# Optimization experiments

Measured on AMD Instinct MI355X. Metric: run time of the kernel, lower is better.

## Reference

```python
import jax, jax.numpy as jnp
import numpy as np

C = 256          # in_channels == out_channels
K = 4            # number of parallel depthwise kernels
RED = 4          # SE reduction
KS = 3           # kernel size


def setup_inputs() -> dict:
    key = jax.random.key(0)
    ks = jax.random.split(key, 6)
    B, H, W = 32, 64, 64
    x = jax.random.normal(ks[0], (B, C, H, W), dtype=jnp.float32)
    # K depthwise kernels; per-conv torch weight shape = (C, 1, 3, 3)
    conv_w = jax.random.normal(ks[1], (K, C, 1, KS, KS), dtype=jnp.float32) * 0.1
    fc1_w = jax.random.normal(ks[2], (C // RED, C), dtype=jnp.float32) * (1.0 / np.sqrt(C))
    fc1_b = jnp.zeros((C // RED,), dtype=jnp.float32)
    fc2_w = jax.random.normal(ks[3], (K, C // RED), dtype=jnp.float32) * (1.0 / np.sqrt(C // RED))
    fc2_b = jnp.zeros((K,), dtype=jnp.float32)
    return {"x": x, "conv_w": conv_w, "fc1_w": fc1_w, "fc1_b": fc1_b,
            "fc2_w": fc2_w, "fc2_b": fc2_b}


def reference(x, conv_w, fc1_w, fc1_b, fc2_w, fc2_b):
    B, c, H, W = x.shape
    # --- attention branch: GAP -> fc -> relu -> fc -> softmax over K ---
    g = jnp.mean(x, axis=(2, 3))                       # [B, C]
    h = jax.nn.relu(g @ fc1_w.T + fc1_b)               # [B, C//r]
    attn = jax.nn.softmax(h @ fc2_w.T + fc2_b, axis=1) # [B, K]
    # --- all K depthwise convs as ONE grouped conv with K*C output channels ---
    # group i (input channel i) produces output channels [i*K:(i+1)*K],
    # so arrange weights as (C, K, 1, ks, ks) -> (C*K, 1, ks, ks)
    w_all = jnp.transpose(conv_w, (1, 0, 2, 3, 4)).reshape(c * K, 1, KS, KS)
    out = jax.lax.conv_general_dilated(
        x, w_all, window_strides=(1, 1), padding=[(1, 1), (1, 1)],
        feature_group_count=c,
        dimension_numbers=("NCHW", "OIHW", "NCHW"))    # [B, C*K, H, W]
    out = out.reshape(B, c, K, H, W)
    # attention-weighted sum over the K kernels
    return jnp.einsum("bckhw,bk->bchw", out, attn)
```

## Files before the change

kernel.cpp:

```cpp
#include <hip/hip_runtime.h>

#define CH 256
#define KK 4
#define HW 64
#define PLANE 4096
#define TILE_W 66

__global__ void gap_kernel(const float* __restrict__ x, float* __restrict__ g) {
    int plane = blockIdx.x;
    const float4* p = (const float4*)(x + (size_t)plane * PLANE);
    float sum = 0.f;
    for (int i = threadIdx.x; i < PLANE / 4; i += 256) {
        float4 v = p[i];
        sum += (v.x + v.y) + (v.z + v.w);
    }
    for (int off = 32; off > 0; off >>= 1)
        sum += __shfl_down(sum, off);
    __shared__ float ws[4];
    int lane = threadIdx.x & 63;
    int wid  = threadIdx.x >> 6;
    if (lane == 0) ws[wid] = sum;
    __syncthreads();
    if (threadIdx.x == 0)
        g[plane] = (ws[0] + ws[1] + ws[2] + ws[3]) * (1.f / PLANE);
}

__global__ void attn_kernel(const float* __restrict__ g,
                            const float* __restrict__ fc1_w, const float* __restrict__ fc1_b,
                            const float* __restrict__ fc2_w, const float* __restrict__ fc2_b,
                            float* __restrict__ attn) {
    int b = blockIdx.x;
    int t = threadIdx.x;
    __shared__ float gs[CH];
    __shared__ float h[64];
    __shared__ float logit[KK];
    for (int i = t; i < CH; i += 64) gs[i] = g[b * CH + i];
    __syncthreads();
    float acc = fc1_b[t];
    const float* wrow = fc1_w + t * CH;
    for (int i = 0; i < CH; ++i) acc = fmaf(wrow[i], gs[i], acc);
    h[t] = fmaxf(acc, 0.f);
    __syncthreads();
    if (t < KK) {
        float a = fc2_b[t];
        const float* w2 = fc2_w + t * 64;
        for (int i = 0; i < 64; ++i) a = fmaf(w2[i], h[i], a);
        logit[t] = a;
    }
    __syncthreads();
    if (t == 0) {
        float m = fmaxf(fmaxf(logit[0], logit[1]), fmaxf(logit[2], logit[3]));
        float e[KK];
        float s = 0.f;
        for (int k = 0; k < KK; ++k) { e[k] = expf(logit[k] - m); s += e[k]; }
        float inv = 1.f / s;
        for (int k = 0; k < KK; ++k) attn[b * KK + k] = e[k] * inv;
    }
}

__global__ void dwconv_kernel(const float* __restrict__ x, const float* __restrict__ conv_w,
                              const float* __restrict__ attn, float* __restrict__ out) {
    int plane = blockIdx.x;
    int b = plane >> 8;
    int c = plane & (CH - 1);
    __shared__ float tile[TILE_W * TILE_W];

    const float* xp = x + (size_t)plane * PLANE;
    for (int i = threadIdx.x; i < TILE_W * TILE_W; i += 256) {
        int sy = i / TILE_W;
        int sx = i - sy * TILE_W;
        int gy = sy - 1, gx = sx - 1;
        float v = 0.f;
        if ((unsigned)gy < 64u && (unsigned)gx < 64u) v = xp[(gy << 6) + gx];
        tile[i] = v;
    }

    float a0 = attn[b * KK + 0], a1 = attn[b * KK + 1],
          a2 = attn[b * KK + 2], a3 = attn[b * KK + 3];
    float w[9];
    #pragma unroll
    for (int j = 0; j < 9; ++j) {
        w[j] = a0 * conv_w[(0 * CH + c) * 9 + j]
             + a1 * conv_w[(1 * CH + c) * 9 + j]
             + a2 * conv_w[(2 * CH + c) * 9 + j]
             + a3 * conv_w[(3 * CH + c) * 9 + j];
    }
    __syncthreads();

    float* op = out + (size_t)plane * PLANE;
    for (int i = threadIdx.x; i < PLANE; i += 256) {
        int y  = i >> 6;
        int xx = i & 63;
        const float* t0 = &tile[y * TILE_W + xx];
        float r = t0[0]            * w[0] + t0[1]            * w[1] + t0[2]            * w[2]
                + t0[TILE_W]       * w[3] + t0[TILE_W + 1]   * w[4] + t0[TILE_W + 2]   * w[5]
                + t0[2 * TILE_W]   * w[6] + t0[2 * TILE_W+1] * w[7] + t0[2 * TILE_W+2] * w[8];
        op[i] = r;
    }
}

extern "C" void kernel_launch(void* const* d_in, const int* in_sizes, int n_in,
                              void* d_out, int out_size, void* d_ws, size_t ws_size,
                              hipStream_t stream) {
    const float* x      = (const float*)d_in[0];
    const float* conv_w = (const float*)d_in[1];
    const float* fc1_w  = (const float*)d_in[2];
    const float* fc1_b  = (const float*)d_in[3];
    const float* fc2_w  = (const float*)d_in[4];
    const float* fc2_b  = (const float*)d_in[5];
    float* out = (float*)d_out;

    int B = in_sizes[0] / (CH * HW * HW);

    float* g    = (float*)d_ws;
    float* attn = g + B * CH;

    gap_kernel <<<B * CH, 256, 0, stream>>>(x, g);
    attn_kernel<<<B, 64, 0, stream>>>(g, fc1_w, fc1_b, fc2_w, fc2_b, attn);
    dwconv_kernel<<<B * CH, 256, 0, stream>>>(x, conv_w, attn, out);
}
```

Before: 286.4 us.

## Vectorize depthwise conv loads/stores, compute 4 outputs per thread, pad tile stride

The depthwise conv kernel now loads the input plane with float4 global reads into a shared tile with row stride 67, and zero-fills only the halo border. Each thread computes four adjacent outputs from shared-memory row segments and writes them with a nontemporal float4 store. This cuts per-element index arithmetic and redundant shared-memory reads, and keeps the streamed output from displacing x in cache. The GAP and attention kernels are also unrolled and vectorized and use a fast exp, though they matter little for total time.

After: 262.4 us. 8.4% less time.

```diff
diff --git a/kernel.cpp b/kernel.cpp
--- a/kernel.cpp
+++ b/kernel.cpp
@@ -4,14 +4,18 @@
 #define KK 4
 #define HW 64
 #define PLANE 4096
-#define TILE_W 66
+#define TS 67
 
-__global__ void gap_kernel(const float* __restrict__ x, float* __restrict__ g) {
+typedef float fx4 __attribute__((ext_vector_type(4)));
+
+__global__ __launch_bounds__(256) void gap_kernel(const float* __restrict__ x,
+                                                  float* __restrict__ g) {
     int plane = blockIdx.x;
     const float4* p = (const float4*)(x + (size_t)plane * PLANE);
     float sum = 0.f;
-    for (int i = threadIdx.x; i < PLANE / 4; i += 256) {
-        float4 v = p[i];
+    #pragma unroll
+    for (int k = 0; k < 4; ++k) {
+        float4 v = p[threadIdx.x + k * 256];
         sum += (v.x + v.y) + (v.z + v.w);
     }
     for (int off = 32; off > 0; off >>= 1)
@@ -25,7 +29,7 @@
         g[plane] = (ws[0] + ws[1] + ws[2] + ws[3]) * (1.f / PLANE);
 }
 
-__global__ void attn_kernel(const float* __restrict__ g,
+__global__ __launch_bounds__(64) void attn_kernel(const float* __restrict__ g,
                             const float* __restrict__ fc1_w, const float* __restrict__ fc1_b,
                             const float* __restrict__ fc2_w, const float* __restrict__ fc2_b,
                             float* __restrict__ attn) {
@@ -36,43 +40,75 @@
     __shared__ float logit[KK];
     for (int i = t; i < CH; i += 64) gs[i] = g[b * CH + i];
     __syncthreads();
-    float acc = fc1_b[t];
-    const float* wrow = fc1_w + t * CH;
-    for (int i = 0; i < CH; ++i) acc = fmaf(wrow[i], gs[i], acc);
-    h[t] = fmaxf(acc, 0.f);
+    {
+        const float4* wr = (const float4*)(fc1_w + t * CH);
+        const float4* gv = (const float4*)gs;
+        float a0 = fc1_b[t], a1 = 0.f, a2 = 0.f, a3 = 0.f;
+        #pragma unroll 4
+        for (int i = 0; i < CH / 4; ++i) {
+            float4 w4 = wr[i], g4 = gv[i];
+            a0 = fmaf(w4.x, g4.x, a0);
+            a1 = fmaf(w4.y, g4.y, a1);
+            a2 = fmaf(w4.z, g4.z, a2);
+            a3 = fmaf(w4.w, g4.w, a3);
+        }
+        h[t] = fmaxf((a0 + a1) + (a2 + a3), 0.f);
+    }
     __syncthreads();
     if (t < KK) {
-        float a = fc2_b[t];
-        const float* w2 = fc2_w + t * 64;
-        for (int i = 0; i < 64; ++i) a = fmaf(w2[i], h[i], a);
-        logit[t] = a;
+        const float4* w2 = (const float4*)(fc2_w + t * 64);
+        const float4* hv = (const float4*)h;
+        float a0 = fc2_b[t], a1 = 0.f, a2 = 0.f, a3 = 0.f;
+        #pragma unroll
+        for (int i = 0; i < 16; ++i) {
+            float4 w4 = w2[i], h4 = hv[i];
+            a0 = fmaf(w4.x, h4.x, a0);
+            a1 = fmaf(w4.y, h4.y, a1);
+            a2 = fmaf(w4.z, h4.z, a2);
+            a3 = fmaf(w4.w, h4.w, a3);
+        }
+        logit[t] = (a0 + a1) + (a2 + a3);
     }
     __syncthreads();
     if (t == 0) {
         float m = fmaxf(fmaxf(logit[0], logit[1]), fmaxf(logit[2], logit[3]));
         float e[KK];
         float s = 0.f;
-        for (int k = 0; k < KK; ++k) { e[k] = expf(logit[k] - m); s += e[k]; }
+        #pragma unroll
+        for (int k = 0; k < KK; ++k) { e[k] = __expf(logit[k] - m); s += e[k]; }
         float inv = 1.f / s;
+        #pragma unroll
         for (int k = 0; k < KK; ++k) attn[b * KK + k] = e[k] * inv;
     }
 }
 
-__global__ void dwconv_kernel(const float* __restrict__ x, const float* __restrict__ conv_w,
+__global__ __launch_bounds__(256) void dwconv_kernel(const float* __restrict__ x,
+                              const float* __restrict__ conv_w,
                               const float* __restrict__ attn, float* __restrict__ out) {
     int plane = blockIdx.x;
     int b = plane >> 8;
     int c = plane & (CH - 1);
-    __shared__ float tile[TILE_W * TILE_W];
+    __shared__ float tile[66 * TS];
+    int t = threadIdx.x;
 
-    const float* xp = x + (size_t)plane * PLANE;
-    for (int i = threadIdx.x; i < TILE_W * TILE_W; i += 256) {
-        int sy = i / TILE_W;
-        int sx = i - sy * TILE_W;
-        int gy = sy - 1, gx = sx - 1;
-        float v = 0.f;
-        if ((unsigned)gy < 64u && (unsigned)gx < 64u) v = xp[(gy << 6) + gx];
-        tile[i] = v;
+    for (int i = t; i < 260; i += 256) {
+        int idx;
+        if (i < 66)       idx = i;
+        else if (i < 132) idx = 65 * TS + (i - 66);
+        else if (i < 196) idx = (i - 131) * TS;
+        else              idx = (i - 195) * TS + 65;
+        tile[idx] = 0.f;
+    }
+
+    const float4* xp4 = (const float4*)(x + (size_t)plane * PLANE);
+    #pragma unroll
+    for (int k = 0; k < 4; ++k) {
+        int idx = t + k * 256;
+        int y   = idx >> 4;
+        int xq  = (idx & 15) << 2;
+        float4 v = xp4[idx];
+        float* d = &tile[(y + 1) * TS + 1 + xq];
+        d[0] = v.x; d[1] = v.y; d[2] = v.z; d[3] = v.w;
     }
 
     float a0 = attn[b * KK + 0], a1 = attn[b * KK + 1],
@@ -87,15 +123,25 @@
     }
     __syncthreads();
 
-    float* op = out + (size_t)plane * PLANE;
-    for (int i = threadIdx.x; i < PLANE; i += 256) {
-        int y  = i >> 6;
-        int xx = i & 63;
-        const float* t0 = &tile[y * TILE_W + xx];
-        float r = t0[0]            * w[0] + t0[1]            * w[1] + t0[2]            * w[2]
-                + t0[TILE_W]       * w[3] + t0[TILE_W + 1]   * w[4] + t0[TILE_W + 2]   * w[5]
-                + t0[2 * TILE_W]   * w[6] + t0[2 * TILE_W+1] * w[7] + t0[2 * TILE_W+2] * w[8];
-        op[i] = r;
+    int y0 = t >> 4;
+    int xq = (t & 15) << 2;
+    fx4* op4 = (fx4*)(out + (size_t)plane * PLANE);
+    #pragma unroll
+    for (int gi = 0; gi < 4; ++gi) {
+        int y = y0 + gi * 16;
+        float s0 = 0.f, s1 = 0.f, s2 = 0.f, s3 = 0.f;
+        #pragma unroll
+        for (int dy = 0; dy < 3; ++dy) {
+            const float* r = &tile[(y + dy) * TS + xq];
+            float e0 = r[0], e1 = r[1], e2 = r[2], e3 = r[3], e4 = r[4], e5 = r[5];
+            float w0 = w[dy * 3], w1 = w[dy * 3 + 1], w2 = w[dy * 3 + 2];
+            s0 = fmaf(e0, w0, fmaf(e1, w1, fmaf(e2, w2, s0)));
+            s1 = fmaf(e1, w0, fmaf(e2, w1, fmaf(e3, w2, s1)));
+            s2 = fmaf(e2, w0, fmaf(e3, w1, fmaf(e4, w2, s2)));
+            s3 = fmaf(e3, w0, fmaf(e4, w1, fmaf(e5, w2, s3)));
+        }
+        fx4 res = {s0, s1, s2, s3};
+        __builtin_nontemporal_store(res, &op4[(y << 4) + (t & 15)]);
     }
 }
 
```
